# Kernel optimization log

Measured on AMD Instinct MI355X. Metric: run time of the kernel, lower is better.

## Reference

```python
import jax, jax.numpy as jnp
import numpy as np
from jax import lax

DIM = 128
K = 3
PAD = K // 2


def setup_inputs() -> dict:
    key = jax.random.key(0)
    k1, k2, k3, k4, k5 = jax.random.split(key, 5)
    B, H, W = 64, 32, 32
    wdim = DIM * DIM * K * K + DIM  # 147584
    # scale question_rep (it encodes conv weights) for numerical sanity
    question_rep = jax.random.normal(k1, (B, wdim), dtype=jnp.float32) * 0.05
    lhs_rep = jax.random.normal(k2, (B, DIM, H, W), dtype=jnp.float32)
    rhs_rep = jax.random.normal(k3, (B, DIM, H, W), dtype=jnp.float32)
    proj_w = jax.random.normal(k4, (DIM, 2 * DIM), dtype=jnp.float32) * (1.0 / np.sqrt(2 * DIM))
    proj_b = jax.random.normal(k5, (DIM,), dtype=jnp.float32) * 0.01
    return {"question_rep": question_rep, "lhs_rep": lhs_rep,
            "rhs_rep": rhs_rep, "proj_w": proj_w, "proj_b": proj_b}


def _per_sample_conv(x, w, b):
    # x: [dim, H, W], w: [dim, dim, K, K], b: [dim]
    y = lax.conv_general_dilated(
        x[None], w, window_strides=(1, 1),
        padding=[(PAD, PAD), (PAD, PAD)],
        dimension_numbers=("NCHW", "OIHW", "NCHW"))
    return y[0] + b[:, None, None]


def reference(question_rep, lhs_rep, rhs_rep, proj_w, proj_b):
    B = question_rep.shape[0]
    wdim = DIM * DIM * K * K
    cnn_weight = question_rep[:, :wdim].reshape(B, DIM, DIM, K, K)
    cnn_bias = question_rep[:, wdim:]  # [B, dim]
    # 1x1 projection conv: cat along channels then contract
    cat = jnp.concatenate([lhs_rep, rhs_rep], axis=1)  # [B, 2*dim, H, W]
    cnn_inp = jnp.einsum("bchw,oc->bohw", cat, proj_w) + proj_b[None, :, None, None]
    # per-sample dynamic conv, vectorized over batch (equiv. grouped conv)
    out = jax.vmap(_per_sample_conv)(cnn_inp, cnn_weight, cnn_bias)
    return out
```

## Files before the change

### kernel.cpp

```cpp
#include <hip/hip_runtime.h>
#include <hip/hip_bf16.h>

#define QSTRIDE 147584
#define WOFF    147456

typedef __attribute__((ext_vector_type(8))) short bf16x8;
typedef __attribute__((ext_vector_type(4))) float f32x4;

static __device__ __forceinline__ ushort f2bf(float f) {
  union { float f; unsigned u; } x; x.f = f;
  unsigned r = x.u + 0x7fffu + ((x.u >> 16) & 1u);
  return (ushort)(r >> 16);
}
static __device__ __forceinline__ unsigned pk2(ushort a, ushort b) {
  return (unsigned)a | ((unsigned)b << 16);
}
static __device__ __forceinline__ void async16(const ushort* g, ushort* l) {
  __builtin_amdgcn_global_load_lds((const __attribute__((address_space(1))) void*)g,
                                   (__attribute__((address_space(3))) void*)l, 16, 0, 0);
}

__global__ __launch_bounds__(256) void pack_w_kernel(const float* __restrict__ q,
                                                     ushort* __restrict__ wt2) {
  int b    = blockIdx.x >> 3;
  int ogrp = blockIdx.x & 7;
  int t    = threadIdx.x;
  int o    = ogrp * 16 + (t >> 4);
  int ci0  = (t & 15) * 8;
  int cq   = ci0 >> 5, coff = ci0 & 31;
  const float* src = q + (size_t)b * QSTRIDE + (size_t)o * 1152 + (size_t)ci0 * 9;
  float v[72];
  const float4* s4 = (const float4*)src;
#pragma unroll
  for (int i = 0; i < 18; ++i) {
    float4 f = s4[i];
    v[4*i+0] = f.x; v[4*i+1] = f.y; v[4*i+2] = f.z; v[4*i+3] = f.w;
  }
  ushort* dstb = wt2 + (size_t)b * 147456 + (size_t)cq * 4096 + o * 32 + coff;
#pragma unroll
  for (int tap = 0; tap < 9; ++tap) {
    ushort u[8];
#pragma unroll
    for (int j = 0; j < 8; ++j) u[j] = f2bf(v[j*9 + tap]);
    uint4 pkv;
    pkv.x = pk2(u[0],u[1]); pkv.y = pk2(u[2],u[3]);
    pkv.z = pk2(u[4],u[5]); pkv.w = pk2(u[6],u[7]);
    *(uint4*)(dstb + (size_t)tap * 16384) = pkv;
  }
}

__global__ __launch_bounds__(256) void pack_pw_kernel(const float* __restrict__ pw,
                                                      ushort* __restrict__ pwb2) {
  int tg = blockIdx.x * 256 + threadIdx.x;
  int o  = tg >> 5;
  int c0 = (tg & 31) * 8;
  const float4* s4 = (const float4*)(pw + (size_t)o * 256 + c0);
  float4 f0 = s4[0], f1 = s4[1];
  uint4 pkv;
  pkv.x = pk2(f2bf(f0.x), f2bf(f0.y)); pkv.y = pk2(f2bf(f0.z), f2bf(f0.w));
  pkv.z = pk2(f2bf(f1.x), f2bf(f1.y)); pkv.w = pk2(f2bf(f1.z), f2bf(f1.w));
  *(uint4*)(pwb2 + (size_t)(c0 >> 5) * 4096 + o * 32 + (c0 & 31)) = pkv;
}

__global__ __launch_bounds__(256) void zero_border_kernel(ushort* __restrict__ xp2) {
  int b = blockIdx.x, t = threadIdx.x;
  for (int idx = t; idx < 528; idx += 256) {
    int cq = idx / 132, r = idx - cq * 132;
    int hp, wp;
    if (r < 34)       { hp = 0;        wp = r; }
    else if (r < 68)  { hp = 33;       wp = r - 34; }
    else if (r < 100) { hp = r - 67;   wp = 0; }
    else              { hp = r - 99;   wp = 33; }
    uint4 z = {0u,0u,0u,0u};
    uint4* dst = (uint4*)(xp2 + (((size_t)b * 4 + cq) * 1156 + hp * 34 + wp) * 32);
#pragma unroll
    for (int i = 0; i < 4; ++i) dst[i] = z;
  }
}

__global__ __launch_bounds__(256, 2) void proj_kernel(const ushort* __restrict__ pwb2,
                                                      const float* __restrict__ lhs,
                                                      const float* __restrict__ rhs,
                                                      const float* __restrict__ pb,
                                                      ushort* __restrict__ xp2) {
  __shared__ ushort As[128 * 32];
  __shared__ ushort Bs[128 * 32];
  int b = blockIdx.y, tile = blockIdx.x;
  int p0 = tile * 128;
  int t = threadIdx.x;
  int lane = t & 63, wv = t >> 6;
  int m0 = (wv & 1) * 64, n0 = (wv >> 1) * 64;
  int quad = lane >> 4, li = lane & 15;
  f32x4 acc[4][4] = {};
  int cgrp = t & 3;
  int pq   = t >> 2;

  for (int c0 = 0; c0 < 256; c0 += 32) {
    const float* src = (c0 < 128 ? lhs : rhs) + (size_t)b * 131072
                     + (size_t)((c0 & 127) + cgrp * 8) * 1024 + p0 + 2 * pq;
    ushort u0[8], u1[8];
#pragma unroll
    for (int j = 0; j < 8; ++j) {
      float2 f = *(const float2*)(src + (size_t)j * 1024);
      u0[j] = f2bf(f.x); u1[j] = f2bf(f.y);
    }
    __syncthreads();
    {
      const ushort* ag = pwb2 + (size_t)(c0 >> 5) * 4096;
      async16(ag + (size_t)wv * 512 + lane * 8,       As + wv * 512);
      async16(ag + (size_t)(wv + 4) * 512 + lane * 8, As + (wv + 4) * 512);
    }
    {
      uint4 pk0, pk1;
      pk0.x = pk2(u0[0],u0[1]); pk0.y = pk2(u0[2],u0[3]);
      pk0.z = pk2(u0[4],u0[5]); pk0.w = pk2(u0[6],u0[7]);
      pk1.x = pk2(u1[0],u1[1]); pk1.y = pk2(u1[2],u1[3]);
      pk1.z = pk2(u1[4],u1[5]); pk1.w = pk2(u1[6],u1[7]);
      *(uint4*)(Bs + (size_t)(2*pq)   * 32 + cgrp * 8) = pk0;
      *(uint4*)(Bs + (size_t)(2*pq+1) * 32 + cgrp * 8) = pk1;
    }
    __syncthreads();
    bf16x8 af[4], bg[4];
#pragma unroll
    for (int mi = 0; mi < 4; ++mi)
      af[mi] = *(const bf16x8*)(As + (m0 + mi*16 + li) * 32 + quad * 8);
#pragma unroll
    for (int ni = 0; ni < 4; ++ni)
      bg[ni] = *(const bf16x8*)(Bs + (n0 + ni*16 + li) * 32 + quad * 8);
#pragma unroll
    for (int mi = 0; mi < 4; ++mi)
#pragma unroll
      for (int ni = 0; ni < 4; ++ni)
        acc[mi][ni] = __builtin_amdgcn_mfma_f32_16x16x32_bf16(af[mi], bg[ni], acc[mi][ni], 0, 0, 0);
  }

  ushort* xpb = xp2 + (size_t)b * 4 * 1156 * 32;
#pragma unroll
  for (int mi = 0; mi < 4; ++mi) {
    int o0 = m0 + mi*16 + quad*4;
    float4 bias = *(const float4*)(pb + o0);
#pragma unroll
    for (int ni = 0; ni < 4; ++ni) {
      int p = p0 + n0 + ni*16 + li;
      int h = p >> 5, w = p & 31;
      ushort* dp = xpb + ((size_t)(o0 >> 5) * 1156 + (h + 1) * 34 + (w + 1)) * 32 + (o0 & 31);
      f32x4 a = acc[mi][ni];
      uint2 pkv;
      pkv.x = pk2(f2bf(a.x + bias.x), f2bf(a.y + bias.y));
      pkv.y = pk2(f2bf(a.z + bias.z), f2bf(a.w + bias.w));
      *(uint2*)dp = pkv;
    }
  }
}

__global__ __launch_bounds__(256, 2) void conv_kernel(const ushort* __restrict__ wt2,
                                                      const ushort* __restrict__ xp2,
                                                      const float* __restrict__ q,
                                                      float* __restrict__ out) {
  __shared__ ushort As[128 * 32];
  __shared__ ushort Bs[128 * 32];
  int b = blockIdx.y, tile = blockIdx.x;
  int p0 = tile * 128, h0 = tile * 4;
  int t = threadIdx.x;
  int lane = t & 63, wv = t >> 6;
  int m0 = (wv & 1) * 64, n0 = (wv >> 1) * 64;
  int quad = lane >> 4, li = lane & 15;
  f32x4 acc[4][4] = {};
  const ushort* wtb = wt2 + (size_t)b * 147456;
  const ushort* xpb = xp2 + (size_t)b * 4 * 1156 * 32;

  for (int tap = 0; tap < 9; ++tap) {
    int kh = tap / 3, kw = tap - kh * 3;
    for (int cq = 0; cq < 4; ++cq) {
      __syncthreads();
      const ushort* ag = wtb + (size_t)(tap * 4 + cq) * 4096;
      async16(ag + (size_t)wv * 512 + lane * 8,       As + wv * 512);
      async16(ag + (size_t)(wv + 4) * 512 + lane * 8, As + (wv + 4) * 512);
      const ushort* bgp = xpb + (size_t)((cq * 1156) + (h0 + wv + kh) * 34 + kw) * 32;
      async16(bgp + lane * 8,       Bs + wv * 1024);
      async16(bgp + 512 + lane * 8, Bs + wv * 1024 + 512);
      __syncthreads();
      bf16x8 af[4], bg[4];
#pragma unroll
      for (int mi = 0; mi < 4; ++mi)
        af[mi] = *(const bf16x8*)(As + (m0 + mi*16 + li) * 32 + quad * 8);
#pragma unroll
      for (int ni = 0; ni < 4; ++ni)
        bg[ni] = *(const bf16x8*)(Bs + (n0 + ni*16 + li) * 32 + quad * 8);
#pragma unroll
      for (int mi = 0; mi < 4; ++mi)
#pragma unroll
        for (int ni = 0; ni < 4; ++ni)
          acc[mi][ni] = __builtin_amdgcn_mfma_f32_16x16x32_bf16(af[mi], bg[ni], acc[mi][ni], 0, 0, 0);
    }
  }

  const float* qb = q + (size_t)b * QSTRIDE + WOFF;
  float* ob = out + (size_t)b * 128 * 1024 + p0;
#pragma unroll
  for (int mi = 0; mi < 4; ++mi) {
    int o0 = m0 + mi*16 + quad*4;
    float4 bias = *(const float4*)(qb + o0);
#pragma unroll
    for (int ni = 0; ni < 4; ++ni) {
      int pl = n0 + ni*16 + li;
      float* dp = ob + (size_t)o0 * 1024 + pl;
      f32x4 a = acc[mi][ni];
      dp[0]    = a.x + bias.x;
      dp[1024] = a.y + bias.y;
      dp[2048] = a.z + bias.z;
      dp[3072] = a.w + bias.w;
    }
  }
}

extern "C" void kernel_launch(void* const* d_in, const int* in_sizes, int n_in,
                              void* d_out, int out_size, void* d_ws, size_t ws_size,
                              hipStream_t stream) {
  const float* q   = (const float*)d_in[0];
  const float* lhs = (const float*)d_in[1];
  const float* rhs = (const float*)d_in[2];
  const float* pw  = (const float*)d_in[3];
  const float* pb  = (const float*)d_in[4];
  float* out = (float*)d_out;

  char* ws = (char*)d_ws;
  ushort* wt2  = (ushort*)(ws);
  ushort* pwb2 = (ushort*)(ws + 18874368);
  ushort* xp2  = (ushort*)(ws + 18939904);

  pack_w_kernel     <<<512, 256, 0, stream>>>(q, wt2);
  pack_pw_kernel    <<<16,  256, 0, stream>>>(pw, pwb2);
  zero_border_kernel<<<64,  256, 0, stream>>>(xp2);
  proj_kernel       <<<dim3(8, 64), 256, 0, stream>>>(pwb2, lhs, rhs, pb, xp2);
  conv_kernel       <<<dim3(8, 64), 256, 0, stream>>>(wt2, xp2, q, out);
}
```

Measured before the change: 198.8 us.

## Reuse halo input tile across conv taps, double-buffer weights, stage weight packing via LDS

The conv kernel now puts the channel-quarter loop outside the tap loop. It loads a 6-row padded halo tile of activations into LDS once per quarter and indexes it with per-tap offsets, so the same window is no longer reloaded for each of the 9 taps. The weight tiles are double-buffered so the next tap's load overlaps the current MFMAs, and the grid is flattened with batch in the low bits. The weight-packing kernel now stages fp32 weights through LDS with coalesced reads before converting to bf16, at the cost of narrower 4-byte stores and extra barriers.

```diff
diff --git a/kernel.cpp b/kernel.cpp
--- a/kernel.cpp
+++ b/kernel.cpp
@@ -22,30 +22,31 @@
 
 __global__ __launch_bounds__(256) void pack_w_kernel(const float* __restrict__ q,
                                                      ushort* __restrict__ wt2) {
-  int b    = blockIdx.x >> 3;
-  int ogrp = blockIdx.x & 7;
-  int t    = threadIdx.x;
-  int o    = ogrp * 16 + (t >> 4);
-  int ci0  = (t & 15) * 8;
-  int cq   = ci0 >> 5, coff = ci0 & 31;
-  const float* src = q + (size_t)b * QSTRIDE + (size_t)o * 1152 + (size_t)ci0 * 9;
-  float v[72];
-  const float4* s4 = (const float4*)src;
-#pragma unroll
-  for (int i = 0; i < 18; ++i) {
-    float4 f = s4[i];
-    v[4*i+0] = f.x; v[4*i+1] = f.y; v[4*i+2] = f.z; v[4*i+3] = f.w;
-  }
-  ushort* dstb = wt2 + (size_t)b * 147456 + (size_t)cq * 4096 + o * 32 + coff;
-#pragma unroll
-  for (int tap = 0; tap < 9; ++tap) {
-    ushort u[8];
-#pragma unroll
-    for (int j = 0; j < 8; ++j) u[j] = f2bf(v[j*9 + tap]);
-    uint4 pkv;
-    pkv.x = pk2(u[0],u[1]); pkv.y = pk2(u[2],u[3]);
-    pkv.z = pk2(u[4],u[5]); pkv.w = pk2(u[6],u[7]);
-    *(uint4*)(dstb + (size_t)tap * 16384) = pkv;
+  __shared__ float Ls[4608];
+  int b = blockIdx.x >> 3, ogrp = blockIdx.x & 7;
+  int t = threadIdx.x;
+  const float* gbase = q + (size_t)b * QSTRIDE + (size_t)ogrp * 16 * 1152;
+  ushort* dstb = wt2 + (size_t)b * 147456;
+  int o_loc = t >> 6;
+  int ci    = (t & 63) * 2;
+  int cq    = ci >> 5, coff = ci & 31;
+  for (int r = 0; r < 4; ++r) {
+    __syncthreads();
+    const float* gs = gbase + r * 4608;
+#pragma unroll
+    for (int i = 0; i < 18; ++i) Ls[i * 256 + t] = gs[i * 256 + t];
+    __syncthreads();
+    int o_full = ogrp * 16 + r * 4 + o_loc;
+    const float* v = Ls + o_loc * 1152 + ci * 9;
+    float a[18];
+#pragma unroll
+    for (int i = 0; i < 18; ++i) a[i] = v[i];
+    ushort* dd = dstb + (size_t)cq * 4096 + o_full * 32 + coff;
+#pragma unroll
+    for (int tap = 0; tap < 9; ++tap) {
+      unsigned pkv = pk2(f2bf(a[tap]), f2bf(a[9 + tap]));
+      *(unsigned*)(dd + (size_t)tap * 16384) = pkv;
+    }
   }
 }
 
@@ -157,9 +158,10 @@
                                                       const ushort* __restrict__ xp2,
                                                       const float* __restrict__ q,
                                                       float* __restrict__ out) {
-  __shared__ ushort As[128 * 32];
-  __shared__ ushort Bs[128 * 32];
-  int b = blockIdx.y, tile = blockIdx.x;
+  __shared__ ushort As[2][4096];
+  __shared__ ushort Bs[6528];
+  int blk = blockIdx.x;
+  int b = blk & 63, tile = blk >> 6;
   int p0 = tile * 128, h0 = tile * 4;
   int t = threadIdx.x;
   int lane = t & 63, wv = t >> 6;
@@ -167,26 +169,43 @@
   int quad = lane >> 4, li = lane & 15;
   f32x4 acc[4][4] = {};
   const ushort* wtb = wt2 + (size_t)b * 147456;
-  const ushort* xpb = xp2 + (size_t)b * 4 * 1156 * 32;
-
-  for (int tap = 0; tap < 9; ++tap) {
-    int kh = tap / 3, kw = tap - kh * 3;
-    for (int cq = 0; cq < 4; ++cq) {
+  const ushort* xpb = xp2 + (size_t)b * 147968;
+
+  for (int cq = 0; cq < 4; ++cq) {
+    __syncthreads();
+    {
+      const ushort* bgp = xpb + (size_t)(cq * 1156 + h0 * 34) * 32;
+#pragma unroll
+      for (int p = 0; p < 3; ++p)
+        async16(bgp + (size_t)(p * 256 + t) * 8, Bs + p * 2048 + wv * 512);
+      if (t < 48)
+        async16(bgp + (size_t)(768 + t) * 8, Bs + 6144);
+    }
+    {
+      const ushort* ag = wtb + (size_t)cq * 4096;
+      async16(ag + (size_t)t * 8,         As[0] + wv * 512);
+      async16(ag + (size_t)(256 + t) * 8, As[0] + 2048 + wv * 512);
+    }
+    for (int tap = 0; tap < 9; ++tap) {
       __syncthreads();
-      const ushort* ag = wtb + (size_t)(tap * 4 + cq) * 4096;
-      async16(ag + (size_t)wv * 512 + lane * 8,       As + wv * 512);
-      async16(ag + (size_t)(wv + 4) * 512 + lane * 8, As + (wv + 4) * 512);
-      const ushort* bgp = xpb + (size_t)((cq * 1156) + (h0 + wv + kh) * 34 + kw) * 32;
-      async16(bgp + lane * 8,       Bs + wv * 1024);
-      async16(bgp + 512 + lane * 8, Bs + wv * 1024 + 512);
-      __syncthreads();
+      if (tap < 8) {
+        const ushort* ag = wtb + (size_t)((tap + 1) * 4 + cq) * 4096;
+        ushort* ab = As[(tap + 1) & 1];
+        async16(ag + (size_t)t * 8,         ab + wv * 512);
+        async16(ag + (size_t)(256 + t) * 8, ab + 2048 + wv * 512);
+      }
+      int kh = tap / 3, kw = tap - kh * 3;
+      const ushort* ar = As[tap & 1];
       bf16x8 af[4], bg[4];
 #pragma unroll
       for (int mi = 0; mi < 4; ++mi)
-        af[mi] = *(const bf16x8*)(As + (m0 + mi*16 + li) * 32 + quad * 8);
-#pragma unroll
-      for (int ni = 0; ni < 4; ++ni)
-        bg[ni] = *(const bf16x8*)(Bs + (n0 + ni*16 + li) * 32 + quad * 8);
+        af[mi] = *(const bf16x8*)(ar + (m0 + mi*16 + li) * 32 + quad * 8);
+#pragma unroll
+      for (int ni = 0; ni < 4; ++ni) {
+        int pl = n0 + ni*16 + li;
+        int h = pl >> 5, w = pl & 31;
+        bg[ni] = *(const bf16x8*)(Bs + ((h + kh) * 34 + (w + kw)) * 32 + quad * 8);
+      }
 #pragma unroll
       for (int mi = 0; mi < 4; ++mi)
 #pragma unroll
@@ -233,5 +252,5 @@
   pack_pw_kernel    <<<16,  256, 0, stream>>>(pw, pwb2);
   zero_border_kernel<<<64,  256, 0, stream>>>(xp2);
   proj_kernel       <<<dim3(8, 64), 256, 0, stream>>>(pwb2, lhs, rhs, pb, xp2);
-  conv_kernel       <<<dim3(8, 64), 256, 0, stream>>>(wt2, xp2, q, out);
-}
+  conv_kernel       <<<512, 256, 0, stream>>>(wt2, xp2, q, out);
+}
```

Result: faster. 181.5 us (-8.7%).
